# Performance work log

Measured on AMD Instinct MI355X. Metric: run time of the kernel, lower is better.

## Reference

```python
import jax, jax.numpy as jnp
import numpy as np

VOCAB, D_MODEL, HIDDEN, NUM_CLASSES = 32000, 512, 768, 2
B, S = 64, 512


def _gru_dir(x_sbd, Wi, Wh, bi, bh, reverse):
    # x_sbd: [S,B,D]; Wi: [3H,D]; Wh: [3H,H]; bi,bh: [3H]
    H = Wh.shape[1]
    xg = jnp.einsum('sbd,gd->sbg', x_sbd, Wi) + bi  # [S,B,3H] precomputed input gates

    def step(h, xg_t):
        hg = h @ Wh.T + bh
        xr, xz, xn = jnp.split(xg_t, 3, axis=-1)
        hr, hz, hn = jnp.split(hg, 3, axis=-1)
        r = jax.nn.sigmoid(xr + hr)
        z = jax.nn.sigmoid(xz + hz)
        n = jnp.tanh(xn + r * hn)
        h_new = (1.0 - z) * n + z * h
        return h_new, None

    h0 = jnp.zeros((x_sbd.shape[1], H), dtype=x_sbd.dtype)
    h_last, _ = jax.lax.scan(step, h0, xg, reverse=reverse)
    return h_last  # [B,H]


def setup_inputs() -> dict:
    key = jax.random.key(0)
    ks = jax.random.split(key, 16)
    sd, sh = 1.0 / np.sqrt(D_MODEL), 1.0 / np.sqrt(HIDDEN)
    inp = {
        'input_ids': jax.random.randint(ks[0], (B, S), 0, VOCAB),
        'emb': jax.random.normal(ks[1], (VOCAB, D_MODEL), jnp.float32),
        'Wi_f': jax.random.uniform(ks[2], (3 * HIDDEN, D_MODEL), jnp.float32, -sd, sd),
        'Wh_f': jax.random.uniform(ks[3], (3 * HIDDEN, HIDDEN), jnp.float32, -sh, sh),
        'bi_f': jax.random.uniform(ks[4], (3 * HIDDEN,), jnp.float32, -sh, sh),
        'bh_f': jax.random.uniform(ks[5], (3 * HIDDEN,), jnp.float32, -sh, sh),
        'Wi_b': jax.random.uniform(ks[6], (3 * HIDDEN, D_MODEL), jnp.float32, -sd, sd),
        'Wh_b': jax.random.uniform(ks[7], (3 * HIDDEN, HIDDEN), jnp.float32, -sh, sh),
        'bi_b': jax.random.uniform(ks[8], (3 * HIDDEN,), jnp.float32, -sh, sh),
        'bh_b': jax.random.uniform(ks[9], (3 * HIDDEN,), jnp.float32, -sh, sh),
        'W1': jax.random.uniform(ks[10], (HIDDEN, 2 * HIDDEN), jnp.float32, -sh, sh),
        'b1': jnp.zeros((HIDDEN,), jnp.float32),
        'W2': jax.random.uniform(ks[11], (NUM_CLASSES, HIDDEN), jnp.float32, -sh, sh),
        'b2': jnp.zeros((NUM_CLASSES,), jnp.float32),
    }
    return inp


def reference(input_ids, emb, Wi_f, Wh_f, bi_f, bh_f, Wi_b, Wh_b, bi_b, bh_b, W1, b1, W2, b2):
    x = emb[input_ids]                      # [B,S,D]
    x_sbd = jnp.transpose(x, (1, 0, 2))     # [S,B,D]
    h_fwd = _gru_dir(x_sbd, Wi_f, Wh_f, bi_f, bh_f, reverse=False)
    h_bwd = _gru_dir(x_sbd, Wi_b, Wh_b, bi_b, bh_b, reverse=True)
    h = jnp.concatenate([h_fwd, h_bwd], axis=-1)  # [B,2H]
    hid = jax.nn.relu(h @ W1.T + b1)
    logits = hid @ W2.T + b2                # [B,num_classes]
    return logits
```

## Files before the change

### kernel.cpp

```cpp
#include <hip/hip_runtime.h>
#include <hip/hip_bf16.h>
#include <cstdint>

typedef _Float16 h2 __attribute__((ext_vector_type(2)));
typedef _Float16 h4 __attribute__((ext_vector_type(4)));
typedef _Float16 h8 __attribute__((ext_vector_type(8)));
typedef float f4 __attribute__((ext_vector_type(4)));
typedef unsigned long long u64;
typedef unsigned int u32;

#define S_LEN 512
#define BATCH 64
#define DM    512
#define HID   768

union h4u { u64 u; h4 v; };

static __device__ __forceinline__ h8 pack8(float4 a, float4 b) {
  h8 v;
  v[0] = (_Float16)a.x; v[1] = (_Float16)a.y;
  v[2] = (_Float16)a.z; v[3] = (_Float16)a.w;
  v[4] = (_Float16)b.x; v[5] = (_Float16)b.y;
  v[6] = (_Float16)b.z; v[7] = (_Float16)b.w;
  return v;
}

static __device__ __forceinline__ h8 ldfrag(const _Float16* S, int row, int ke) {
  int byte = (row << 7) + (ke << 1);
  byte ^= (row & 7) << 4;
  return *(const h8*)((const char*)S + byte);
}
static __device__ __forceinline__ void stfrag(_Float16* S, int row, int ke, h8 v) {
  int byte = (row << 7) + (ke << 1);
  byte ^= (row & 7) << 4;
  *(h8*)((char*)S + byte) = v;
}

__global__ __launch_bounds__(256) void gemm1_kernel(
    const int* __restrict__ ids, const float* __restrict__ emb,
    const float* __restrict__ Wi_f, const float* __restrict__ bi_f,
    const float* __restrict__ Wi_b, const float* __restrict__ bi_b,
    int s0_f, int s0_b,
    _Float16* __restrict__ xg_f, _Float16* __restrict__ xg_b)
{
  const int mt  = blockIdx.x;
  const int nt  = blockIdx.y;
  const int dir = blockIdx.z;
  const float* __restrict__ Wi = dir ? Wi_b : Wi_f;
  const float* __restrict__ bi = dir ? bi_b : bi_f;
  _Float16*   __restrict__ xg  = dir ? xg_b : xg_f;
  const int s0 = dir ? s0_b : s0_f;

  __shared__ _Float16 Ws[128 * 64];
  __shared__ _Float16 Es[128 * 64];
  __shared__ int ids_s[128];

  const int tid = threadIdx.x;
  if (tid < 128) {
    ids_s[tid] = ids[(tid & 63) * S_LEN + s0 + mt * 2 + (tid >> 6)];
  }

  const int w  = tid >> 6;
  const int L  = tid & 63;
  const int lh = L >> 4;
  const int ln = L & 15;
  const int wn = (w >> 1) * 64;
  const int wm = (w & 1) * 64;

  const int r  = tid >> 1;
  const int kh = (tid & 1) * 32;

  f4 acc[4][4];
#pragma unroll
  for (int i = 0; i < 4; ++i)
#pragma unroll
    for (int j = 0; j < 4; ++j) { acc[i][j][0]=0.f; acc[i][j][1]=0.f; acc[i][j][2]=0.f; acc[i][j][3]=0.f; }

  __syncthreads();

  for (int kt = 0; kt < DM; kt += 64) {
    {
      const float* srcW = Wi + (size_t)(nt * 128 + r) * DM + kt + kh;
      const float* srcE = emb + (size_t)ids_s[r] * DM + kt + kh;
      float4 w0 = ((const float4*)srcW)[0], w1 = ((const float4*)srcW)[1];
      float4 w2 = ((const float4*)srcW)[2], w3 = ((const float4*)srcW)[3];
      float4 w4 = ((const float4*)srcW)[4], w5 = ((const float4*)srcW)[5];
      float4 w6 = ((const float4*)srcW)[6], w7 = ((const float4*)srcW)[7];
      float4 e0 = ((const float4*)srcE)[0], e1 = ((const float4*)srcE)[1];
      float4 e2 = ((const float4*)srcE)[2], e3 = ((const float4*)srcE)[3];
      float4 e4 = ((const float4*)srcE)[4], e5 = ((const float4*)srcE)[5];
      float4 e6 = ((const float4*)srcE)[6], e7 = ((const float4*)srcE)[7];
      stfrag(Ws, r, kh + 0,  pack8(w0, w1));
      stfrag(Ws, r, kh + 8,  pack8(w2, w3));
      stfrag(Ws, r, kh + 16, pack8(w4, w5));
      stfrag(Ws, r, kh + 24, pack8(w6, w7));
      stfrag(Es, r, kh + 0,  pack8(e0, e1));
      stfrag(Es, r, kh + 8,  pack8(e2, e3));
      stfrag(Es, r, kh + 16, pack8(e4, e5));
      stfrag(Es, r, kh + 24, pack8(e6, e7));
    }
    __syncthreads();
#pragma unroll
    for (int ks = 0; ks < 2; ++ks) {
      h8 af[4], bf[4];
#pragma unroll
      for (int i = 0; i < 4; ++i) af[i] = ldfrag(Ws, wn + i * 16 + ln, ks * 32 + lh * 8);
#pragma unroll
      for (int j = 0; j < 4; ++j) bf[j] = ldfrag(Es, wm + j * 16 + ln, ks * 32 + lh * 8);
#pragma unroll
      for (int i = 0; i < 4; ++i)
#pragma unroll
        for (int j = 0; j < 4; ++j)
          acc[i][j] = __builtin_amdgcn_mfma_f32_16x16x32_f16(af[i], bf[j], acc[i][j], 0, 0, 0);
    }
    __syncthreads();
  }

#pragma unroll
  for (int i = 0; i < 4; ++i) {
    const int n_g = nt * 128 + wn + i * 16 + lh * 4;
    const int gate = n_g / 768;
    const int jj = n_g - gate * 768;
    const f4 bv = *(const f4*)&bi[n_g];
#pragma unroll
    for (int j = 0; j < 4; ++j) {
      const int m = mt * 128 + wm + j * 16 + ln;
      const int sl = m >> 6, b = m & 63;
      h4 v;
#pragma unroll
      for (int rr = 0; rr < 4; ++rr) v[rr] = (_Float16)(acc[i][j][rr] + bv[rr]);
      *(h4*)&xg[(((size_t)sl * 3 + gate) * 64 + b) * 768 + jj] = v;
    }
  }
}

__global__ __launch_bounds__(256, 1) void scan_mfma_kernel(
    const float* __restrict__ Wh_f, const float* __restrict__ bh_f,
    const float* __restrict__ Wh_b, const float* __restrict__ bh_b,
    const _Float16* __restrict__ xg_f, const _Float16* __restrict__ xg_b,
    char* __restrict__ hx,
    float* __restrict__ hfin,
    int step0, int nsteps)
{
  const int blk = blockIdx.x;
  const int dir = blk / 48;
  const int l   = blk - dir * 48;
  const int bg  = l / 12;
  const int jb  = l - bg * 12;

  const float* __restrict__ Wh = dir ? Wh_b : Wh_f;
  const float* __restrict__ bh = dir ? bh_b : bh_f;
  const _Float16* __restrict__ xg = dir ? xg_b : xg_f;
  char*  payB = hx + (size_t)dir * 2 * 64 * 1536;
  float* hfd  = hfin + (size_t)dir * 64 * 768;

  const int tid = threadIdx.x;
  const int w   = tid >> 6;
  const int L   = tid & 63;
  const int lh  = L >> 4;
  const int ln  = L & 15;
  const int jt  = jb * 4 + w;
  const int jrow = jt * 16 + ln;
  const int j0l  = jt * 16 + lh * 4;
  const int bglob = bg * 16 + ln;
  const int bb  = tid >> 4;
  const int qi  = tid & 15;

  __shared__ __align__(16) unsigned char hs[96 * 256];

  h8 A[3][24];
#pragma unroll
  for (int g = 0; g < 3; ++g)
#pragma unroll
    for (int ks = 0; ks < 24; ++ks) {
      const float* src = Wh + (size_t)(g * 768 + jrow) * 768 + ks * 32 + lh * 8;
      float4 w0 = ((const float4*)src)[0];
      float4 w1 = ((const float4*)src)[1];
      A[g][ks] = pack8(w0, w1);
    }

  f4 bhv[3];
#pragma unroll
  for (int g = 0; g < 3; ++g) bhv[g] = *(const f4*)&bh[g * 768 + j0l];

  f4 hm;
  if (step0 == 0) { hm[0]=0.f; hm[1]=0.f; hm[2]=0.f; hm[3]=0.f; }
  else {
    const float* src = &hfd[(size_t)bglob * 768 + j0l];
    asm volatile("global_load_dwordx4 %0, %1, off sc0 sc1\n\t"
                 "s_waitcnt vmcnt(0)"
                 : "=&v"(hm) : "v"(src) : "memory");
  }

  char* const pslot = payB + (size_t)bglob * 1536 + (size_t)(jt * 4 + lh) * 8;
  const char* const crow = payB + (size_t)(bg * 16 + bb) * 1536 + qi * 16;
  const int swb = (bb ^ (qi & 7)) * 16;

  for (int t = 0; t < nsteps; ++t) {
    const int sg = step0 + t;
    const int pin = sg & 1, pout = pin ^ 1;

    const int lsl = dir ? (nsteps - 1 - t) : t;
    const _Float16* xrow = xg + (((size_t)lsl * 3) * 64 + bglob) * 768 + j0l;
    h4 xr4 = *(const h4*)xrow;
    h4 xz4 = *(const h4*)(xrow + (size_t)64 * 768);
    h4 xn4 = *(const h4*)(xrow + (size_t)2 * 64 * 768);

    const u32 texp = (u32)sg & 15u;
    const u32 e0 = ((texp & 1u) << 14) | ((texp & 2u) << 29);
    const u32 e1 = ((texp & 4u) << 12) | ((texp & 8u) << 27);
    const char* pc = crow + (size_t)pin * 64 * 1536;
    u64 q0,q1,q2,q3,q4,q5,q6,q7,q8,q9,q10,q11;
    for (;;) {
      asm volatile(
        "global_load_dwordx2 %0, %12, off sc0 sc1\n\t"
        "global_load_dwordx2 %1, %12, off offset:8 sc0 sc1\n\t"
        "global_load_dwordx2 %2, %13, off sc0 sc1\n\t"
        "global_load_dwordx2 %3, %13, off offset:8 sc0 sc1\n\t"
        "global_load_dwordx2 %4, %14, off sc0 sc1\n\t"
        "global_load_dwordx2 %5, %14, off offset:8 sc0 sc1\n\t"
        "global_load_dwordx2 %6, %15, off sc0 sc1\n\t"
        "global_load_dwordx2 %7, %15, off offset:8 sc0 sc1\n\t"
        "global_load_dwordx2 %8, %16, off sc0 sc1\n\t"
        "global_load_dwordx2 %9, %16, off offset:8 sc0 sc1\n\t"
        "global_load_dwordx2 %10, %17, off sc0 sc1\n\t"
        "global_load_dwordx2 %11, %17, off offset:8 sc0 sc1\n\t"
        "s_waitcnt vmcnt(0)"
        : "=&v"(q0), "=&v"(q1), "=&v"(q2), "=&v"(q3), "=&v"(q4), "=&v"(q5),
          "=&v"(q6), "=&v"(q7), "=&v"(q8), "=&v"(q9), "=&v"(q10), "=&v"(q11)
        : "v"(pc), "v"(pc + 256), "v"(pc + 512),
          "v"(pc + 768), "v"(pc + 1024), "v"(pc + 1280)
        : "memory");
      u32 bad = 0;
      u64 qs[12] = {q0,q1,q2,q3,q4,q5,q6,q7,q8,q9,q10,q11};
#pragma unroll
      for (int i = 0; i < 12; ++i) {
        u32 lo = (u32)qs[i], hi = (u32)(qs[i] >> 32);
        bad |= ((lo & 0x40004000u) ^ e0) | ((hi & 0x40004000u) ^ e1);
      }
      if (bad == 0) break;
    }
    {
      const u64 CM = 0xBFFFBFFFBFFFBFFFull;
      u64 qa[12] = {q0&CM,q1&CM,q2&CM,q3&CM,q4&CM,q5&CM,q6&CM,q7&CM,q8&CM,q9&CM,q10&CM,q11&CM};
#pragma unroll
      for (int i = 0; i < 6; ++i) {
        u64* d = (u64*)(hs + (qi + 16 * i) * 256 + swb);
        d[0] = qa[2 * i];
        d[1] = qa[2 * i + 1];
      }
    }
    __syncthreads();

    f4 Cr, Cz, Cn;
    Cr[0]=0.f;Cr[1]=0.f;Cr[2]=0.f;Cr[3]=0.f;
    Cz = Cr; Cn = Cr;
#pragma unroll
    for (int ks = 0; ks < 24; ++ks) {
      const int p = ks * 4 + lh;
      h8 Bf = *(const h8*)(hs + p * 256 + ((ln ^ (p & 7)) * 16));
      Cr = __builtin_amdgcn_mfma_f32_16x16x32_f16(A[0][ks], Bf, Cr, 0, 0, 0);
      Cz = __builtin_amdgcn_mfma_f32_16x16x32_f16(A[1][ks], Bf, Cz, 0, 0, 0);
      Cn = __builtin_amdgcn_mfma_f32_16x16x32_f16(A[2][ks], Bf, Cn, 0, 0, 0);
    }

    f4 hnew;
    h4u st;
#pragma unroll
    for (int r = 0; r < 4; ++r) {
      float rr = 1.f / (1.f + __expf(-((float)xr4[r] + Cr[r] + bhv[0][r])));
      float zz = 1.f / (1.f + __expf(-((float)xz4[r] + Cz[r] + bhv[1][r])));
      float nn = tanhf((float)xn4[r] + rr * (Cn[r] + bhv[2][r]));
      hnew[r] = (1.f - zz) * nn + zz * hm[r];
      st.v[r] = (_Float16)fminf(1.f, fmaxf(-1.f, hnew[r]));
    }
    hm = hnew;

    {
      const u32 tw = (u32)(sg + 1) & 15u;
      u32 lo = (u32)st.u, hi = (u32)(st.u >> 32);
      lo |= ((tw & 1u) << 14) | ((tw & 2u) << 29);
      hi |= ((tw & 4u) << 12) | ((tw & 8u) << 27);
      u64 pv = ((u64)hi << 32) | lo;
      char* dst = pslot + (size_t)pout * 64 * 1536;
      asm volatile("global_store_dwordx2 %0, %1, off sc0 sc1"
                   :: "v"(dst), "v"(pv) : "memory");
    }
    __syncthreads();
  }

  {
    float* dst = &hfd[(size_t)bglob * 768 + j0l];
    asm volatile("global_store_dwordx4 %0, %1, off sc0 sc1"
                 :: "v"(dst), "v"(hm) : "memory");
  }
}

__global__ __launch_bounds__(256) void mlp1_kernel(
    const float* __restrict__ hfin, const float* __restrict__ W1,
    const float* __restrict__ b1, float* __restrict__ hid)
{
  const int c = blockIdx.x * 4 + (threadIdx.x >> 6);
  const int b = threadIdx.x & 63;
  const float* __restrict__ hf = hfin + (size_t)b * 768;
  const float* __restrict__ hb = hfin + (size_t)(64 + b) * 768;
  const float* __restrict__ w = W1 + (size_t)c * 1536;
  float acc = b1[c];
  for (int k = 0; k < 768; k += 4) {
    float4 hv = *(const float4*)&hf[k];
    float4 wv = *(const float4*)&w[k];
    acc += hv.x * wv.x + hv.y * wv.y + hv.z * wv.z + hv.w * wv.w;
  }
  for (int k = 0; k < 768; k += 4) {
    float4 hv = *(const float4*)&hb[k];
    float4 wv = *(const float4*)&w[768 + k];
    acc += hv.x * wv.x + hv.y * wv.y + hv.z * wv.z + hv.w * wv.w;
  }
  hid[(size_t)c * 64 + b] = fmaxf(acc, 0.f);
}

__global__ void mlp2_kernel(const float* __restrict__ hid,
                            const float* __restrict__ W2,
                            const float* __restrict__ b2,
                            float* __restrict__ out)
{
  const int tid = threadIdx.x;
  const int b = tid & 63, cls = tid >> 6;
  const float* __restrict__ w = W2 + cls * 768;
  float acc = b2[cls];
  for (int k = 0; k < 768; ++k) acc += hid[(size_t)k * 64 + b] * w[k];
  out[b * 2 + cls] = acc;
}

extern "C" void kernel_launch(void* const* d_in, const int* in_sizes, int n_in,
                              void* d_out, int out_size, void* d_ws, size_t ws_size,
                              hipStream_t stream)
{
  const int*   ids  = (const int*)d_in[0];
  const float* emb  = (const float*)d_in[1];
  const float* Wi_f = (const float*)d_in[2];
  const float* Wh_f = (const float*)d_in[3];
  const float* bi_f = (const float*)d_in[4];
  const float* bh_f = (const float*)d_in[5];
  const float* Wi_b = (const float*)d_in[6];
  const float* Wh_b = (const float*)d_in[7];
  const float* bi_b = (const float*)d_in[8];
  const float* bh_b = (const float*)d_in[9];
  const float* W1   = (const float*)d_in[10];
  const float* b1   = (const float*)d_in[11];
  const float* W2   = (const float*)d_in[12];
  const float* b2   = (const float*)d_in[13];
  float* out = (float*)d_out;

  const size_t B_HX   = (size_t)2 * 2 * 64 * 1536;
  const size_t B_HFIN = (size_t)2 * 64 * 768 * 4;
  const size_t B_HID  = (size_t)HID * BATCH * 4;
  const size_t state_bytes = B_HX + B_HFIN + B_HID;

  int CH = 512;
  while (CH > 8) {
    size_t need = (size_t)4 * CH * 64 * 2304 + state_bytes;
    if (need <= ws_size) break;
    CH >>= 1;
  }
  const size_t SZ_XG = (size_t)CH * 64 * 2304;

  char* ws = (char*)d_ws;
  _Float16* xg_f = (_Float16*)ws;
  _Float16* xg_b = xg_f + SZ_XG;
  char*     hx   = (char*)(xg_b + SZ_XG);
  float*    hfin = (float*)(hx + B_HX);
  float*    hid  = (float*)((char*)hfin + B_HFIN);

  (void)hipMemsetAsync(hx, 0, state_bytes, stream);

  const int nch = 512 / CH;
  for (int c = 0; c < nch; ++c) {
    const int s0f = c * CH;
    const int s0b = 512 - (c + 1) * CH;
    gemm1_kernel<<<dim3(CH / 2, 18, 2), 256, 0, stream>>>(
        ids, emb, Wi_f, bi_f, Wi_b, bi_b, s0f, s0b, xg_f, xg_b);
    scan_mfma_kernel<<<96, 256, 0, stream>>>(
        Wh_f, bh_f, Wh_b, bh_b, xg_f, xg_b, hx, hfin, c * CH, CH);
  }
  mlp1_kernel<<<192, 256, 0, stream>>>(hfin, W1, b1, hid);
  mlp2_kernel<<<1, 128, 0, stream>>>(hid, W2, b2, out);
}
```

Before: 2.593 ms.

## Overlap next-chunk input-gate GEMM with current scan via fused launch

```diff
diff --git a/kernel.cpp b/kernel.cpp
--- a/kernel.cpp
+++ b/kernel.cpp
@@ -36,24 +36,22 @@
   *(h8*)((char*)S + byte) = v;
 }
 
-__global__ __launch_bounds__(256) void gemm1_kernel(
+static __device__ void gemm_body(
+    unsigned char* smem, int mt, int nt, int dir,
     const int* __restrict__ ids, const float* __restrict__ emb,
     const float* __restrict__ Wi_f, const float* __restrict__ bi_f,
     const float* __restrict__ Wi_b, const float* __restrict__ bi_b,
     int s0_f, int s0_b,
     _Float16* __restrict__ xg_f, _Float16* __restrict__ xg_b)
 {
-  const int mt  = blockIdx.x;
-  const int nt  = blockIdx.y;
-  const int dir = blockIdx.z;
   const float* __restrict__ Wi = dir ? Wi_b : Wi_f;
   const float* __restrict__ bi = dir ? bi_b : bi_f;
   _Float16*   __restrict__ xg  = dir ? xg_b : xg_f;
   const int s0 = dir ? s0_b : s0_f;
 
-  __shared__ _Float16 Ws[128 * 64];
-  __shared__ _Float16 Es[128 * 64];
-  __shared__ int ids_s[128];
+  _Float16* Ws = (_Float16*)smem;
+  _Float16* Es = (_Float16*)(smem + 16384);
+  int* ids_s   = (int*)(smem + 32768);
 
   const int tid = threadIdx.x;
   if (tid < 128) {
@@ -134,15 +132,26 @@
   }
 }
 
-__global__ __launch_bounds__(256, 1) void scan_mfma_kernel(
+__global__ __launch_bounds__(256) void gemm1_kernel(
+    const int* __restrict__ ids, const float* __restrict__ emb,
+    const float* __restrict__ Wi_f, const float* __restrict__ bi_f,
+    const float* __restrict__ Wi_b, const float* __restrict__ bi_b,
+    int s0_f, int s0_b,
+    _Float16* __restrict__ xg_f, _Float16* __restrict__ xg_b)
+{
+  __shared__ __align__(16) unsigned char smem[33280];
+  gemm_body(smem, blockIdx.x, blockIdx.y, blockIdx.z,
+            ids, emb, Wi_f, bi_f, Wi_b, bi_b, s0_f, s0_b, xg_f, xg_b);
+}
+
+static __device__ void scan_body(
+    unsigned char* hs, int blk,
     const float* __restrict__ Wh_f, const float* __restrict__ bh_f,
     const float* __restrict__ Wh_b, const float* __restrict__ bh_b,
     const _Float16* __restrict__ xg_f, const _Float16* __restrict__ xg_b,
-    char* __restrict__ hx,
-    float* __restrict__ hfin,
+    char* __restrict__ hx, float* __restrict__ hfin,
     int step0, int nsteps)
 {
-  const int blk = blockIdx.x;
   const int dir = blk / 48;
   const int l   = blk - dir * 48;
   const int bg  = l / 12;
@@ -165,8 +174,6 @@
   const int bglob = bg * 16 + ln;
   const int bb  = tid >> 4;
   const int qi  = tid & 15;
-
-  __shared__ __align__(16) unsigned char hs[96 * 256];
 
   h8 A[3][24];
 #pragma unroll
@@ -296,6 +303,33 @@
   }
 }
 
+__global__ __launch_bounds__(256, 1) void fused_kernel(
+    const float* __restrict__ Wh_f, const float* __restrict__ bh_f,
+    const float* __restrict__ Wh_b, const float* __restrict__ bh_b,
+    const _Float16* __restrict__ sxg_f, const _Float16* __restrict__ sxg_b,
+    char* __restrict__ hx, float* __restrict__ hfin, int step0, int nsteps,
+    const int* __restrict__ ids, const float* __restrict__ emb,
+    const float* __restrict__ Wi_f, const float* __restrict__ bi_f,
+    const float* __restrict__ Wi_b, const float* __restrict__ bi_b,
+    int g_s0f, int g_s0b,
+    _Float16* __restrict__ gxg_f, _Float16* __restrict__ gxg_b, int mtc)
+{
+  __shared__ __align__(16) unsigned char smem[33280];
+  const int b = blockIdx.x;
+  if (b < 96) {
+    scan_body(smem, b, Wh_f, bh_f, Wh_b, bh_b, sxg_f, sxg_b,
+              hx, hfin, step0, nsteps);
+  } else {
+    const int e = b - 96;
+    const int mt = e % mtc;
+    const int r2 = e / mtc;
+    const int nt = r2 % 18;
+    const int dir = r2 / 18;
+    gemm_body(smem, mt, nt, dir, ids, emb, Wi_f, bi_f, Wi_b, bi_b,
+              g_s0f, g_s0b, gxg_f, gxg_b);
+  }
+}
+
 __global__ __launch_bounds__(256) void mlp1_kernel(
     const float* __restrict__ hfin, const float* __restrict__ W1,
     const float* __restrict__ b1, float* __restrict__ hid)
@@ -359,29 +393,33 @@
 
   int CH = 512;
   while (CH > 8) {
-    size_t need = (size_t)4 * CH * 64 * 2304 + state_bytes;
+    size_t need = (size_t)8 * CH * 64 * 2304 + state_bytes;
     if (need <= ws_size) break;
     CH >>= 1;
   }
   const size_t SZ_XG = (size_t)CH * 64 * 2304;
 
   char* ws = (char*)d_ws;
-  _Float16* xg_f = (_Float16*)ws;
-  _Float16* xg_b = xg_f + SZ_XG;
-  char*     hx   = (char*)(xg_b + SZ_XG);
+  _Float16* xgbuf0 = (_Float16*)ws;
+  _Float16* xgbuf1 = xgbuf0 + 2 * SZ_XG;
+  char*     hx   = (char*)(xgbuf1 + 2 * SZ_XG);
   float*    hfin = (float*)(hx + B_HX);
   float*    hid  = (float*)((char*)hfin + B_HFIN);
 
   (void)hipMemsetAsync(hx, 0, state_bytes, stream);
 
   const int nch = 512 / CH;
+  gemm1_kernel<<<dim3(CH / 2, 18, 2), 256, 0, stream>>>(
+      ids, emb, Wi_f, bi_f, Wi_b, bi_b, 0, 512 - CH, xgbuf0, xgbuf0 + SZ_XG);
+
   for (int c = 0; c < nch; ++c) {
-    const int s0f = c * CH;
-    const int s0b = 512 - (c + 1) * CH;
-    gemm1_kernel<<<dim3(CH / 2, 18, 2), 256, 0, stream>>>(
-        ids, emb, Wi_f, bi_f, Wi_b, bi_b, s0f, s0b, xg_f, xg_b);
-    scan_mfma_kernel<<<96, 256, 0, stream>>>(
-        Wh_f, bh_f, Wh_b, bh_b, xg_f, xg_b, hx, hfin, c * CH, CH);
+    _Float16* sf = (c & 1) ? xgbuf1 : xgbuf0;
+    _Float16* gf = (c & 1) ? xgbuf0 : xgbuf1;
+    const int ng = (c + 1 < nch) ? (CH / 2) * 36 : 0;
+    fused_kernel<<<96 + ng, 256, 0, stream>>>(
+        Wh_f, bh_f, Wh_b, bh_b, sf, sf + SZ_XG, hx, hfin, c * CH, CH,
+        ids, emb, Wi_f, bi_f, Wi_b, bi_b,
+        (c + 1) * CH, 512 - (c + 2) * CH, gf, gf + SZ_XG, CH / 2);
   }
   mlp1_kernel<<<192, 256, 0, stream>>>(hfin, W1, b1, hid);
   mlp2_kernel<<<1, 128, 0, stream>>>(hid, W2, b2, out);
```

Measured after the change: 2.366 ms. 1.1x faster.
